# Performance work log

Measured on AMD Instinct MI355X. Metric: run time of the kernel, lower is better.

## Reference

```python
import jax, jax.numpy as jnp
import numpy as np

NUM_EXPERTS = 8
TOP_K = 2


def setup_inputs() -> dict:
    key = jax.random.key(0)
    k1, k2, k3, k4, k5 = jax.random.split(key, 5)
    B, S, H, F, E = 4, 1024, 1024, 2048, NUM_EXPERTS
    return {
        "hidden_states": jax.random.normal(k1, (B, S, H), dtype=jnp.float32),
        "gate_w": jax.random.normal(k2, (H, E), dtype=jnp.float32) * 0.02,
        "w1": jax.random.normal(k3, (E, H, F), dtype=jnp.float32) * 0.02,
        "w2": jax.random.normal(k4, (E, F, H), dtype=jnp.float32) * 0.02,
        "w3": jax.random.normal(k5, (E, H, F), dtype=jnp.float32) * 0.02,
    }


def reference(hidden_states, gate_w, w1, w2, w3):
    """Mixtral MoE block: router softmax -> top-2 -> SwiGLU expert FFN -> weighted combine.

    Same math as Gmm (sort + grouped GEMM + scatter): each token passes through its
    top-k experts' FFNs (silu(x@w1) * (x@w3)) @ w2, then the outputs are combined
    with the renormalized top-k routing weights.
    """
    B, S, H = hidden_states.shape
    E = w1.shape[0]
    x = hidden_states.reshape(-1, H)                       # [m, H]
    m = x.shape[0]

    router_logits = x @ gate_w                             # [m, E]
    probs = jax.nn.softmax(router_logits, axis=-1)
    top_w, top_i = jax.lax.top_k(probs, TOP_K)             # [m, k]
    top_w = top_w / jnp.sum(top_w, axis=-1, keepdims=True)

    # dense routing matrix [m, E] (top-k indices are distinct per row)
    route = jnp.zeros((m, E), dtype=x.dtype)
    route = route.at[jnp.arange(m)[:, None], top_i].set(top_w)

    out = jnp.zeros_like(x)
    for e in range(E):  # fixed small expert count; accumulate to keep memory low
        h = jax.nn.silu(x @ w1[e]) * (x @ w3[e])           # [m, F]
        out = out + route[:, e:e + 1] * (h @ w2[e])        # [m, H]

    return out.reshape(B, S, H)
```

## Files before the change

### kernel.cpp

```cpp
#include <hip/hip_runtime.h>

typedef __attribute__((ext_vector_type(8))) short bf16x8;
typedef __attribute__((ext_vector_type(4))) float f32x4;

#define MTOK 4096
#define HD 1024
#define FD 2048
#define NEXP 8
#define MAXT 72

struct Ctl {
  int counts[NEXP];
  int cursor[NEXP];
  int totalTiles;
  int _pad[7];
  int4 tileMap[MAXT];
  int topE[MTOK][2];
  float topW[MTOK][2];
  int pos[MTOK][2];
  int rowTok[2 * MTOK];
};

__device__ __forceinline__ unsigned short f2bf(float f) {
  unsigned int u = __float_as_uint(f);
  unsigned int r = u + 0x7fffu + ((u >> 16) & 1u);
  return (unsigned short)(r >> 16);
}
__device__ __forceinline__ float bf2f(unsigned short s) {
  return __uint_as_float(((unsigned int)s) << 16);
}
__device__ __forceinline__ unsigned int pk2(float a, float b) {
  return (unsigned int)f2bf(a) | ((unsigned int)f2bf(b) << 16);
}
__device__ __forceinline__ void gload16(const void* g, void* l) {
  __builtin_amdgcn_global_load_lds(
      (const __attribute__((address_space(1))) void*)g,
      (__attribute__((address_space(3))) void*)l, 16, 0, 0);
}

__global__ void k_tr(const float* __restrict__ in, unsigned short* __restrict__ outp,
                     int K, int N) {
  __shared__ float tile[64][65];
  int ntn = N >> 6, ntk = K >> 6;
  int bid = blockIdx.x;
  int e = bid / (ntk * ntn);
  int rem = bid % (ntk * ntn);
  int kt = rem / ntn, nt = rem % ntn;
  const float* src = in + (size_t)e * K * N + (size_t)(kt * 64) * N + nt * 64;
  unsigned short* dst = outp + (size_t)e * N * K + (size_t)(nt * 64) * K + kt * 64;
  int t = threadIdx.x;
  int nl = t & 63, kq = t >> 6;
#pragma unroll
  for (int i = 0; i < 16; i++) {
    int kl = kq * 16 + i;
    tile[kl][nl] = src[(size_t)kl * N + nl];
  }
  __syncthreads();
  int n2 = t >> 2, kc = (t & 3) * 16;
  unsigned int pk[8];
#pragma unroll
  for (int j = 0; j < 8; j++)
    pk[j] = pk2(tile[kc + 2 * j][n2], tile[kc + 2 * j + 1][n2]);
  *(uint4*)(dst + (size_t)n2 * K + kc) = make_uint4(pk[0], pk[1], pk[2], pk[3]);
  *(uint4*)(dst + (size_t)n2 * K + kc + 8) = make_uint4(pk[4], pk[5], pk[6], pk[7]);
}

__global__ void k_cvt_x(const float* __restrict__ x, unsigned short* __restrict__ xb) {
  int i = blockIdx.x * 256 + threadIdx.x;
  const float4* s = (const float4*)x;
  float4 a = s[i * 2], b = s[i * 2 + 1];
  *(uint4*)(xb + (size_t)i * 8) =
      make_uint4(pk2(a.x, a.y), pk2(a.z, a.w), pk2(b.x, b.y), pk2(b.z, b.w));
}

__global__ void k_router(const float* __restrict__ x, const float* __restrict__ gw,
                         Ctl* __restrict__ ctl) {
  int gt = blockIdx.x * 256 + threadIdx.x;
  int tok = gt >> 6;
  int lane = gt & 63;
  const float* xr = x + (size_t)tok * HD;
  float acc[NEXP] = {};
#pragma unroll
  for (int it = 0; it < 4; it++) {
    int h0 = it * 256 + lane * 4;
    float4 xv = *(const float4*)(xr + h0);
    float xs[4] = {xv.x, xv.y, xv.z, xv.w};
#pragma unroll
    for (int j = 0; j < 4; j++) {
      float4 g0 = *(const float4*)(gw + (size_t)(h0 + j) * 8);
      float4 g1 = *(const float4*)(gw + (size_t)(h0 + j) * 8 + 4);
      acc[0] += xs[j] * g0.x; acc[1] += xs[j] * g0.y;
      acc[2] += xs[j] * g0.z; acc[3] += xs[j] * g0.w;
      acc[4] += xs[j] * g1.x; acc[5] += xs[j] * g1.y;
      acc[6] += xs[j] * g1.z; acc[7] += xs[j] * g1.w;
    }
  }
#pragma unroll
  for (int off = 32; off > 0; off >>= 1) {
#pragma unroll
    for (int e = 0; e < NEXP; e++) acc[e] += __shfl_xor(acc[e], off);
  }
  if (lane == 0) {
    float l0 = -1e30f, l1 = -1e30f; int i0 = 0, i1 = 0;
#pragma unroll
    for (int e = 0; e < NEXP; e++) {
      float v = acc[e];
      if (v > l0) { l1 = l0; i1 = i0; l0 = v; i0 = e; }
      else if (v > l1) { l1 = v; i1 = e; }
    }
    float w0 = 1.f / (1.f + __expf(l1 - l0));
    ctl->topE[tok][0] = i0; ctl->topE[tok][1] = i1;
    ctl->topW[tok][0] = w0; ctl->topW[tok][1] = 1.f - w0;
  }
}

__global__ void k_count(Ctl* __restrict__ ctl) {
  __shared__ int lcnt[NEXP];
  int t = threadIdx.x;
  if (t < NEXP) lcnt[t] = 0;
  __syncthreads();
  int tok = blockIdx.x * 512 + t;
  atomicAdd(&lcnt[ctl->topE[tok][0]], 1);
  atomicAdd(&lcnt[ctl->topE[tok][1]], 1);
  __syncthreads();
  if (t < NEXP && lcnt[t]) atomicAdd(&ctl->counts[t], lcnt[t]);
}

__global__ void k_setup(Ctl* __restrict__ ctl) {
  if (threadIdx.x == 0 && blockIdx.x == 0) {
    int off = 0, t = 0;
    for (int e = 0; e < NEXP; e++) {
      ctl->cursor[e] = off;
      int c = ctl->counts[e];
      int nt = (c + 127) >> 7;
      for (int i = 0; i < nt; i++) {
        if (t < MAXT)
          ctl->tileMap[t] = make_int4(e, off + i * 128, min(128, c - i * 128), 0);
        t++;
      }
      off += c;
    }
    ctl->totalTiles = t;
    for (; t < MAXT; t++) ctl->tileMap[t] = make_int4(0, 0, 0, 0);
  }
}

__global__ void k_scatter(Ctl* __restrict__ ctl) {
  __shared__ int lcur[NEXP];
  __shared__ int gbase[NEXP];
  int t = threadIdx.x;
  int tok = blockIdx.x * 512 + t;
  if (t < NEXP) lcur[t] = 0;
  __syncthreads();
  int e0 = ctl->topE[tok][0];
  int e1 = ctl->topE[tok][1];
  int r0 = atomicAdd(&lcur[e0], 1);
  int r1 = atomicAdd(&lcur[e1], 1);
  __syncthreads();
  if (t < NEXP) gbase[t] = lcur[t] ? atomicAdd(&ctl->cursor[t], lcur[t]) : 0;
  __syncthreads();
  int p0 = gbase[e0] + r0;
  int p1 = gbase[e1] + r1;
  ctl->rowTok[p0] = tok; ctl->pos[tok][0] = p0;
  ctl->rowTok[p1] = tok; ctl->pos[tok][1] = p1;
}

__launch_bounds__(512, 2)
__global__ void k_gemm1(const unsigned short* __restrict__ xb,
                        const unsigned short* __restrict__ w1t,
                        const unsigned short* __restrict__ w3t,
                        unsigned short* __restrict__ hg,
                        const Ctl* __restrict__ ctl) {
  __shared__ __align__(1024) unsigned char lds[2][3][8192];
  int nwg = MAXT * (FD / 128);
  int bid = blockIdx.x;
  int swz = (bid & 7) * (nwg >> 3) + (bid >> 3);
  int rt = swz % MAXT, ct = swz / MAXT;
  int4 tm = ctl->tileMap[rt];
  if (tm.z == 0) return;
  int e = tm.x, grow0 = tm.y, nrows = tm.z;
  int t = threadIdx.x;

  int r = t >> 2;
  int cl = (t & 3) ^ ((r >> 1) & 3);
  int rA = min(r, nrows - 1);
  int tok = ctl->rowTok[grow0 + rA];
  const unsigned short* aG  = xb  + (size_t)tok * HD + cl * 8;
  const unsigned short* b1G = w1t + ((size_t)e * FD + ct * 128 + r) * HD + cl * 8;
  const unsigned short* b3G = w3t + ((size_t)e * FD + ct * 128 + r) * HD + cl * 8;
  unsigned char* ldsDstA  = &lds[0][0][t * 16];
  unsigned char* ldsDstB1 = &lds[0][1][t * 16];
  unsigned char* ldsDstB3 = &lds[0][2][t * 16];

  int lane = t & 63, wv = t >> 6, wr = wv >> 2, wc = wv & 3;
  int lm = lane & 15, lk = lane >> 4;
  int aOff[4], bOff[2];
#pragma unroll
  for (int ma = 0; ma < 4; ma++) {
    int row = wr * 64 + ma * 16 + lm;
    aOff[ma] = row * 64 + ((lk ^ ((row >> 1) & 3)) << 4);
  }
#pragma unroll
  for (int nb = 0; nb < 2; nb++) {
    int row = wc * 32 + nb * 16 + lm;
    bOff[nb] = row * 64 + ((lk ^ ((row >> 1) & 3)) << 4);
  }

  f32x4 accA[4][2] = {};
  f32x4 accC[4][2] = {};

  const int NK = HD / 32;
  gload16(aG, ldsDstA); gload16(b1G, ldsDstB1); gload16(b3G, ldsDstB3);
  for (int kt = 0; kt < NK; kt++) {
    int b = kt & 1;
    if (kt + 1 < NK) {
      size_t ko = (size_t)(kt + 1) * 32;
      int nbuf = b ^ 1;
      gload16(aG + ko,  ldsDstA  + nbuf * 3 * 8192);
      gload16(b1G + ko, ldsDstB1 + nbuf * 3 * 8192);
      gload16(b3G + ko, ldsDstB3 + nbuf * 3 * 8192);
      asm volatile("s_waitcnt vmcnt(3)" ::: "memory");
    } else {
      asm volatile("s_waitcnt vmcnt(0)" ::: "memory");
    }
    __builtin_amdgcn_s_barrier();
    asm volatile("" ::: "memory");
    const unsigned char* pA  = &lds[b][0][0];
    const unsigned char* pB1 = &lds[b][1][0];
    const unsigned char* pB3 = &lds[b][2][0];
    bf16x8 af[4], bf1[2], bf3[2];
#pragma unroll
    for (int ma = 0; ma < 4; ma++) af[ma] = *(const bf16x8*)(pA + aOff[ma]);
#pragma unroll
    for (int nb = 0; nb < 2; nb++) {
      bf1[nb] = *(const bf16x8*)(pB1 + bOff[nb]);
      bf3[nb] = *(const bf16x8*)(pB3 + bOff[nb]);
    }
#pragma unroll
    for (int nb = 0; nb < 2; nb++)
#pragma unroll
      for (int ma = 0; ma < 4; ma++) {
        accA[ma][nb] = __builtin_amdgcn_mfma_f32_16x16x32_bf16(af[ma], bf1[nb], accA[ma][nb], 0, 0, 0);
        accC[ma][nb] = __builtin_amdgcn_mfma_f32_16x16x32_bf16(af[ma], bf3[nb], accC[ma][nb], 0, 0, 0);
      }
    asm volatile("" ::: "memory");
    __builtin_amdgcn_s_barrier();
  }

#pragma unroll
  for (int ma = 0; ma < 4; ma++) {
    int lrowBase = wr * 64 + ma * 16 + lk * 4;
#pragma unroll
    for (int nb = 0; nb < 2; nb++) {
      int col = ct * 128 + wc * 32 + nb * 16 + lm;
#pragma unroll
      for (int rr = 0; rr < 4; rr++) {
        int lrow = lrowBase + rr;
        if (lrow < nrows) {
          float a = accA[ma][nb][rr];
          float c = accC[ma][nb][rr];
          float hv = a / (1.f + __expf(-a)) * c;
          hg[(size_t)(grow0 + lrow) * FD + col] = f2bf(hv);
        }
      }
    }
  }
}

__launch_bounds__(512, 2)
__global__ void k_gemm2(const unsigned short* __restrict__ hg,
                        const unsigned short* __restrict__ w2t,
                        unsigned short* __restrict__ og,
                        const Ctl* __restrict__ ctl) {
  __shared__ __align__(1024) unsigned char lds[2][2][8192];
  int nwg = MAXT * (HD / 128);
  int bid = blockIdx.x;
  int swz = (bid & 7) * (nwg >> 3) + (bid >> 3);
  int rt = swz % MAXT, ct = swz / MAXT;
  int4 tm = ctl->tileMap[rt];
  if (tm.z == 0) return;
  int e = tm.x, grow0 = tm.y, nrows = tm.z;
  int t = threadIdx.x;

  int r = t >> 2;
  int cl = (t & 3) ^ ((r >> 1) & 3);
  int rA = min(r, nrows - 1);
  const unsigned short* aG = hg  + (size_t)(grow0 + rA) * FD + cl * 8;
  const unsigned short* bG = w2t + ((size_t)e * HD + ct * 128 + r) * FD + cl * 8;
  unsigned char* ldsDstA = &lds[0][0][t * 16];
  unsigned char* ldsDstB = &lds[0][1][t * 16];

  int lane = t & 63, wv = t >> 6, wr = wv >> 2, wc = wv & 3;
  int lm = lane & 15, lk = lane >> 4;
  int aOff[4], bOff[2];
#pragma unroll
  for (int ma = 0; ma < 4; ma++) {
    int row = wr * 64 + ma * 16 + lm;
    aOff[ma] = row * 64 + ((lk ^ ((row >> 1) & 3)) << 4);
  }
#pragma unroll
  for (int nb = 0; nb < 2; nb++) {
    int row = wc * 32 + nb * 16 + lm;
    bOff[nb] = row * 64 + ((lk ^ ((row >> 1) & 3)) << 4);
  }

  f32x4 acc[4][2] = {};
  const int NK = FD / 32;
  gload16(aG, ldsDstA); gload16(bG, ldsDstB);
  for (int kt = 0; kt < NK; kt++) {
    int b = kt & 1;
    if (kt + 1 < NK) {
      size_t ko = (size_t)(kt + 1) * 32;
      int nbuf = b ^ 1;
      gload16(aG + ko, ldsDstA + nbuf * 2 * 8192);
      gload16(bG + ko, ldsDstB + nbuf * 2 * 8192);
      asm volatile("s_waitcnt vmcnt(2)" ::: "memory");
    } else {
      asm volatile("s_waitcnt vmcnt(0)" ::: "memory");
    }
    __builtin_amdgcn_s_barrier();
    asm volatile("" ::: "memory");
    const unsigned char* pA = &lds[b][0][0];
    const unsigned char* pB = &lds[b][1][0];
    bf16x8 af[4], bfr[2];
#pragma unroll
    for (int ma = 0; ma < 4; ma++) af[ma] = *(const bf16x8*)(pA + aOff[ma]);
#pragma unroll
    for (int nb = 0; nb < 2; nb++) bfr[nb] = *(const bf16x8*)(pB + bOff[nb]);
#pragma unroll
    for (int nb = 0; nb < 2; nb++)
#pragma unroll
      for (int ma = 0; ma < 4; ma++)
        acc[ma][nb] = __builtin_amdgcn_mfma_f32_16x16x32_bf16(af[ma], bfr[nb], acc[ma][nb], 0, 0, 0);
    asm volatile("" ::: "memory");
    __builtin_amdgcn_s_barrier();
  }

#pragma unroll
  for (int ma = 0; ma < 4; ma++) {
    int lrowBase = wr * 64 + ma * 16 + lk * 4;
#pragma unroll
    for (int nb = 0; nb < 2; nb++) {
      int col = ct * 128 + wc * 32 + nb * 16 + lm;
#pragma unroll
      for (int rr = 0; rr < 4; rr++) {
        int lrow = lrowBase + rr;
        if (lrow < nrows)
          og[(size_t)(grow0 + lrow) * HD + col] = f2bf(acc[ma][nb][rr]);
      }
    }
  }
}

__global__ void k_combine(const unsigned short* __restrict__ og, float* __restrict__ out,
                          const Ctl* __restrict__ ctl) {
  int tok = blockIdx.x;
  int tid = threadIdx.x;
  int p0 = ctl->pos[tok][0], p1 = ctl->pos[tok][1];
  float w0 = ctl->topW[tok][0], w1 = ctl->topW[tok][1];
  uint2 a = *(const uint2*)(og + (size_t)p0 * HD + tid * 4);
  uint2 b = *(const uint2*)(og + (size_t)p1 * HD + tid * 4);
  float4 o;
  o.x = w0 * bf2f((unsigned short)(a.x & 0xffffu)) + w1 * bf2f((unsigned short)(b.x & 0xffffu));
  o.y = w0 * bf2f((unsigned short)(a.x >> 16))     + w1 * bf2f((unsigned short)(b.x >> 16));
  o.z = w0 * bf2f((unsigned short)(a.y & 0xffffu)) + w1 * bf2f((unsigned short)(b.y & 0xffffu));
  o.w = w0 * bf2f((unsigned short)(a.y >> 16))     + w1 * bf2f((unsigned short)(b.y >> 16));
  *(float4*)(out + (size_t)tok * HD + tid * 4) = o;
}

extern "C" void kernel_launch(void* const* d_in, const int* in_sizes, int n_in,
                              void* d_out, int out_size, void* d_ws, size_t ws_size,
                              hipStream_t stream) {
  const float* x  = (const float*)d_in[0];
  const float* gw = (const float*)d_in[1];
  const float* w1 = (const float*)d_in[2];
  const float* w2 = (const float*)d_in[3];
  const float* w3 = (const float*)d_in[4];
  float* out = (float*)d_out;

  char* ws = (char*)d_ws;
  unsigned short* hg  = (unsigned short*)(ws);
  unsigned short* og  = (unsigned short*)(ws + (size_t)(32u << 20));
  unsigned short* xb  = (unsigned short*)(ws + (size_t)(48u << 20));
  unsigned short* wAt = (unsigned short*)(ws + (size_t)(56u << 20));
  unsigned short* wBt = (unsigned short*)(ws + (size_t)(88u << 20));
  Ctl* ctl = (Ctl*)(ws + (size_t)(120u << 20));

  hipMemsetAsync(ctl->counts, 0, sizeof(int) * NEXP, stream);
  k_tr<<<dim3(8 * 16 * 32), 256, 0, stream>>>(w1, wAt, HD, FD);
  k_tr<<<dim3(8 * 16 * 32), 256, 0, stream>>>(w3, wBt, HD, FD);
  k_cvt_x<<<dim3(2048), 256, 0, stream>>>(x, xb);
  k_router<<<dim3(MTOK / 4), 256, 0, stream>>>(x, gw, ctl);
  k_count<<<dim3(MTOK / 512), 512, 0, stream>>>(ctl);
  k_setup<<<1, 64, 0, stream>>>(ctl);
  k_scatter<<<dim3(MTOK / 512), 512, 0, stream>>>(ctl);
  k_gemm1<<<dim3(MAXT * (FD / 128)), 512, 0, stream>>>(xb, wAt, wBt, hg, ctl);
  k_tr<<<dim3(8 * 32 * 16), 256, 0, stream>>>(w2, wAt, FD, HD);
  k_gemm2<<<dim3(MAXT * (HD / 128)), 512, 0, stream>>>(hg, wAt, og, ctl);
  k_combine<<<dim3(MTOK), 256, 0, stream>>>(og, out, ctl);
}
```

Baseline: 400.6 us.

## Triple-buffer LDS in expert GEMMs and vectorize weight transpose loads

Both grouped GEMM kernels move from double to triple LDS buffering, issuing global-to-LDS loads two k-steps ahead with matching vmcnt waits and a peeled epilogue. This is meant to hide more global memory latency behind the MFMA work. The weight transpose kernel now reads float4 vectors with a padded tile row stride. The extra LDS per block (72KB for gemm1) may cut occupancy under launch_bounds(512,2). The modulo-3 buffer indices and the macros' loops without unroll pragmas may also add overhead.

```diff
diff --git a/kernel.cpp b/kernel.cpp
--- a/kernel.cpp
+++ b/kernel.cpp
@@ -40,7 +40,7 @@
 
 __global__ void k_tr(const float* __restrict__ in, unsigned short* __restrict__ outp,
                      int K, int N) {
-  __shared__ float tile[64][65];
+  __shared__ float tile[64][68];
   int ntn = N >> 6, ntk = K >> 6;
   int bid = blockIdx.x;
   int e = bid / (ntk * ntn);
@@ -49,11 +49,12 @@
   const float* src = in + (size_t)e * K * N + (size_t)(kt * 64) * N + nt * 64;
   unsigned short* dst = outp + (size_t)e * N * K + (size_t)(nt * 64) * K + kt * 64;
   int t = threadIdx.x;
-  int nl = t & 63, kq = t >> 6;
-#pragma unroll
-  for (int i = 0; i < 16; i++) {
-    int kl = kq * 16 + i;
-    tile[kl][nl] = src[(size_t)kl * N + nl];
+  int nl4 = t & 15, kr = t >> 4;
+#pragma unroll
+  for (int i = 0; i < 4; i++) {
+    int row = kr + i * 16;
+    float4 v = *(const float4*)(src + (size_t)row * N + nl4 * 4);
+    *(float4*)&tile[row][nl4 * 4] = v;
   }
   __syncthreads();
   int n2 = t >> 2, kc = (t & 3) * 16;
@@ -171,7 +172,7 @@
                         const unsigned short* __restrict__ w3t,
                         unsigned short* __restrict__ hg,
                         const Ctl* __restrict__ ctl) {
-  __shared__ __align__(1024) unsigned char lds[2][3][8192];
+  __shared__ __align__(1024) unsigned char lds[3][3][8192];
   int nwg = MAXT * (FD / 128);
   int bid = blockIdx.x;
   int swz = (bid & 7) * (nwg >> 3) + (bid >> 3);
@@ -210,42 +211,55 @@
   f32x4 accC[4][2] = {};
 
   const int NK = HD / 32;
-  gload16(aG, ldsDstA); gload16(b1G, ldsDstB1); gload16(b3G, ldsDstB3);
-  for (int kt = 0; kt < NK; kt++) {
-    int b = kt & 1;
-    if (kt + 1 < NK) {
-      size_t ko = (size_t)(kt + 1) * 32;
-      int nbuf = b ^ 1;
-      gload16(aG + ko,  ldsDstA  + nbuf * 3 * 8192);
-      gload16(b1G + ko, ldsDstB1 + nbuf * 3 * 8192);
-      gload16(b3G + ko, ldsDstB3 + nbuf * 3 * 8192);
-      asm volatile("s_waitcnt vmcnt(3)" ::: "memory");
-    } else {
-      asm volatile("s_waitcnt vmcnt(0)" ::: "memory");
-    }
+#define G1_STAGE(kt_, buf_)                                            \
+  {                                                                    \
+    size_t ko_ = (size_t)(kt_) * 32;                                   \
+    gload16(aG + ko_,  ldsDstA  + (buf_) * 3 * 8192);                  \
+    gload16(b1G + ko_, ldsDstB1 + (buf_) * 3 * 8192);                  \
+    gload16(b3G + ko_, ldsDstB3 + (buf_) * 3 * 8192);                  \
+  }
+#define G1_COMPUTE(buf_)                                               \
+  {                                                                    \
+    const unsigned char* pA  = &lds[buf_][0][0];                       \
+    const unsigned char* pB1 = &lds[buf_][1][0];                       \
+    const unsigned char* pB3 = &lds[buf_][2][0];                       \
+    bf16x8 af[4], bf1[2], bf3[2];                                      \
+    for (int ma = 0; ma < 4; ma++) af[ma] = *(const bf16x8*)(pA + aOff[ma]); \
+    for (int nb = 0; nb < 2; nb++) {                                   \
+      bf1[nb] = *(const bf16x8*)(pB1 + bOff[nb]);                      \
+      bf3[nb] = *(const bf16x8*)(pB3 + bOff[nb]);                      \
+    }                                                                  \
+    for (int nb = 0; nb < 2; nb++)                                     \
+      for (int ma = 0; ma < 4; ma++) {                                 \
+        accA[ma][nb] = __builtin_amdgcn_mfma_f32_16x16x32_bf16(af[ma], bf1[nb], accA[ma][nb], 0, 0, 0); \
+        accC[ma][nb] = __builtin_amdgcn_mfma_f32_16x16x32_bf16(af[ma], bf3[nb], accC[ma][nb], 0, 0, 0); \
+      }                                                                \
+  }
+
+  G1_STAGE(0, 0);
+  G1_STAGE(1, 1);
+  for (int kt = 0; kt < NK - 2; kt++) {
+    int bc = kt % 3, bn = (kt + 2) % 3;
+    G1_STAGE(kt + 2, bn);
+    asm volatile("s_waitcnt vmcnt(6)" ::: "memory");
     __builtin_amdgcn_s_barrier();
     asm volatile("" ::: "memory");
-    const unsigned char* pA  = &lds[b][0][0];
-    const unsigned char* pB1 = &lds[b][1][0];
-    const unsigned char* pB3 = &lds[b][2][0];
-    bf16x8 af[4], bf1[2], bf3[2];
-#pragma unroll
-    for (int ma = 0; ma < 4; ma++) af[ma] = *(const bf16x8*)(pA + aOff[ma]);
-#pragma unroll
-    for (int nb = 0; nb < 2; nb++) {
-      bf1[nb] = *(const bf16x8*)(pB1 + bOff[nb]);
-      bf3[nb] = *(const bf16x8*)(pB3 + bOff[nb]);
-    }
-#pragma unroll
-    for (int nb = 0; nb < 2; nb++)
-#pragma unroll
-      for (int ma = 0; ma < 4; ma++) {
-        accA[ma][nb] = __builtin_amdgcn_mfma_f32_16x16x32_bf16(af[ma], bf1[nb], accA[ma][nb], 0, 0, 0);
-        accC[ma][nb] = __builtin_amdgcn_mfma_f32_16x16x32_bf16(af[ma], bf3[nb], accC[ma][nb], 0, 0, 0);
-      }
+    G1_COMPUTE(bc);
     asm volatile("" ::: "memory");
     __builtin_amdgcn_s_barrier();
   }
+  asm volatile("s_waitcnt vmcnt(3)" ::: "memory");
+  __builtin_amdgcn_s_barrier();
+  asm volatile("" ::: "memory");
+  G1_COMPUTE((NK - 2) % 3);
+  asm volatile("" ::: "memory");
+  __builtin_amdgcn_s_barrier();
+  asm volatile("s_waitcnt vmcnt(0)" ::: "memory");
+  __builtin_amdgcn_s_barrier();
+  asm volatile("" ::: "memory");
+  G1_COMPUTE((NK - 1) % 3);
+#undef G1_STAGE
+#undef G1_COMPUTE
 
 #pragma unroll
   for (int ma = 0; ma < 4; ma++) {
@@ -272,7 +286,7 @@
                         const unsigned short* __restrict__ w2t,
                         unsigned short* __restrict__ og,
                         const Ctl* __restrict__ ctl) {
-  __shared__ __align__(1024) unsigned char lds[2][2][8192];
+  __shared__ __align__(1024) unsigned char lds[3][2][8192];
   int nwg = MAXT * (HD / 128);
   int bid = blockIdx.x;
   int swz = (bid & 7) * (nwg >> 3) + (bid >> 3);
@@ -306,35 +320,48 @@
 
   f32x4 acc[4][2] = {};
   const int NK = FD / 32;
-  gload16(aG, ldsDstA); gload16(bG, ldsDstB);
-  for (int kt = 0; kt < NK; kt++) {
-    int b = kt & 1;
-    if (kt + 1 < NK) {
-      size_t ko = (size_t)(kt + 1) * 32;
-      int nbuf = b ^ 1;
-      gload16(aG + ko, ldsDstA + nbuf * 2 * 8192);
-      gload16(bG + ko, ldsDstB + nbuf * 2 * 8192);
-      asm volatile("s_waitcnt vmcnt(2)" ::: "memory");
-    } else {
-      asm volatile("s_waitcnt vmcnt(0)" ::: "memory");
-    }
+#define G2_STAGE(kt_, buf_)                                            \
+  {                                                                    \
+    size_t ko_ = (size_t)(kt_) * 32;                                   \
+    gload16(aG + ko_, ldsDstA + (buf_) * 2 * 8192);                    \
+    gload16(bG + ko_, ldsDstB + (buf_) * 2 * 8192);                    \
+  }
+#define G2_COMPUTE(buf_)                                               \
+  {                                                                    \
+    const unsigned char* pA = &lds[buf_][0][0];                        \
+    const unsigned char* pB = &lds[buf_][1][0];                        \
+    bf16x8 af[4], bfr[2];                                              \
+    for (int ma = 0; ma < 4; ma++) af[ma] = *(const bf16x8*)(pA + aOff[ma]); \
+    for (int nb = 0; nb < 2; nb++) bfr[nb] = *(const bf16x8*)(pB + bOff[nb]); \
+    for (int nb = 0; nb < 2; nb++)                                     \
+      for (int ma = 0; ma < 4; ma++)                                   \
+        acc[ma][nb] = __builtin_amdgcn_mfma_f32_16x16x32_bf16(af[ma], bfr[nb], acc[ma][nb], 0, 0, 0); \
+  }
+
+  G2_STAGE(0, 0);
+  G2_STAGE(1, 1);
+  for (int kt = 0; kt < NK - 2; kt++) {
+    int bc = kt % 3, bn = (kt + 2) % 3;
+    G2_STAGE(kt + 2, bn);
+    asm volatile("s_waitcnt vmcnt(4)" ::: "memory");
     __builtin_amdgcn_s_barrier();
     asm volatile("" ::: "memory");
-    const unsigned char* pA = &lds[b][0][0];
-    const unsigned char* pB = &lds[b][1][0];
-    bf16x8 af[4], bfr[2];
-#pragma unroll
-    for (int ma = 0; ma < 4; ma++) af[ma] = *(const bf16x8*)(pA + aOff[ma]);
-#pragma unroll
-    for (int nb = 0; nb < 2; nb++) bfr[nb] = *(const bf16x8*)(pB + bOff[nb]);
-#pragma unroll
-    for (int nb = 0; nb < 2; nb++)
-#pragma unroll
-      for (int ma = 0; ma < 4; ma++)
-        acc[ma][nb] = __builtin_amdgcn_mfma_f32_16x16x32_bf16(af[ma], bfr[nb], acc[ma][nb], 0, 0, 0);
+    G2_COMPUTE(bc);
     asm volatile("" ::: "memory");
     __builtin_amdgcn_s_barrier();
   }
+  asm volatile("s_waitcnt vmcnt(2)" ::: "memory");
+  __builtin_amdgcn_s_barrier();
+  asm volatile("" ::: "memory");
+  G2_COMPUTE((NK - 2) % 3);
+  asm volatile("" ::: "memory");
+  __builtin_amdgcn_s_barrier();
+  asm volatile("s_waitcnt vmcnt(0)" ::: "memory");
+  __builtin_amdgcn_s_barrier();
+  asm volatile("" ::: "memory");
+  G2_COMPUTE((NK - 1) % 3);
+#undef G2_STAGE
+#undef G2_COMPUTE
 
 #pragma unroll
   for (int ma = 0; ma < 4; ma++) {
```

New measurement: 409.6 us. 1.02x slower.
